# Optimization experiments

Measured on AMD Instinct MI355X. Metric: run time of the kernel, lower is better.

## Reference

```python
import jax, jax.numpy as jnp
import numpy as np

N, D, H, F = 384, 512, 8, 64  # n_nodes, in/out features, heads, per-head hidden
SLOPE = 0.2


def gat_v2_layer(x, mask, W_l, W_r, a):
    """GATv2 layer (is_concat=True). x: [N, D_in]; mask: [N, N, 1] bool.

    torch semantics: g_sum[i, j] = g_l[j] + g_r[i]; e = a . LeakyReLU(g_sum);
    softmax over j (dim=1); aggregate g_r with einsum('ijh,jhf->ihf').
    attn linear nn.Linear(F, 1) is shared across heads -> a: [F].
    """
    n = x.shape[0]
    g_l = (x @ W_l).reshape(n, H, F)
    g_r = (x @ W_r).reshape(n, H, F)
    # pairwise [i, j, h, f] = g_r[i] + g_l[j]  (the big O(N^2) intermediate)
    s = jax.nn.leaky_relu(g_r[:, None] + g_l[None, :], negative_slope=SLOPE)
    e = jnp.einsum('ijhf,f->ijh', s, a)
    e = jnp.where(mask, e, -jnp.inf)
    att = jax.nn.softmax(e, axis=1)  # normalize over source nodes j
    out = jnp.einsum('ijh,jhf->ihf', att, g_r)
    return out.reshape(n, H * F)


def setup_inputs() -> dict:
    key = jax.random.key(0)
    ks = jax.random.split(key, 8)
    x = jax.random.normal(ks[0], (N, D), dtype=jnp.float32)
    adj = jax.random.randint(ks[1], (N, N, 1), 0, 2, dtype=jnp.int32)
    sd = 1.0 / np.sqrt(D)
    sa = 1.0 / np.sqrt(F)
    W_l0 = jax.random.normal(ks[2], (D, H * F), dtype=jnp.float32) * sd
    W_r0 = jax.random.normal(ks[3], (D, H * F), dtype=jnp.float32) * sd
    a0 = jax.random.normal(ks[4], (F,), dtype=jnp.float32) * sa
    W_l1 = jax.random.normal(ks[5], (H * F, H * F), dtype=jnp.float32) * sd
    W_r1 = jax.random.normal(ks[6], (H * F, H * F), dtype=jnp.float32) * sd
    a1 = jax.random.normal(ks[7], (F,), dtype=jnp.float32) * sa
    return {"x": x, "adj": adj, "W_l0": W_l0, "W_r0": W_r0, "a0": a0,
            "W_l1": W_l1, "W_r1": W_r1, "a1": a1}


def reference(x, adj, W_l0, W_r0, a0, W_l1, W_r1, a1):
    n = x.shape[0]
    # selfloop: fill diagonal of adj with 1
    idx = jnp.arange(n)
    adj = adj.at[idx, idx, 0].set(1)
    mask = adj != 0  # [N, N, 1]
    # layer 0: GATv2 -> ELU (i < n_layers-1) -> residual
    out = jax.nn.elu(gat_v2_layer(x, mask, W_l0, W_r0, a0))
    x = x + out
    # layer 1: GATv2 -> Identity -> residual
    out = gat_v2_layer(x, mask, W_l1, W_r1, a1)
    x = x + out
    return x
```

## Files before the change

### kernel.cpp

```cpp
#include <hip/hip_runtime.h>
#include <hip/hip_bf16.h>
#include <stdint.h>

typedef unsigned short ushort_t;
typedef unsigned long long u64;
typedef __attribute__((ext_vector_type(8))) short short8;
typedef __attribute__((ext_vector_type(4))) float f32x4;

#define N_NODES 384
#define HF      512

__device__ inline ushort_t f2bf(float f) {
  __hip_bfloat16 b = __float2bfloat16(f);
  return *reinterpret_cast<ushort_t*>(&b);
}
__device__ inline float bf2f_u(ushort_t u) {
  union { float f; uint32_t i; } v; v.i = ((uint32_t)u) << 16; return v.f;
}

__global__ __launch_bounds__(256) void prep(
    const float* __restrict__ x, const int* __restrict__ adj,
    const float* __restrict__ w0, const float* __restrict__ w1,
    const float* __restrict__ w2, const float* __restrict__ w3,
    ushort_t* __restrict__ WT0, ushort_t* __restrict__ WT1,
    ushort_t* __restrict__ xb, u64* __restrict__ mbits)
{
  const int z = blockIdx.z;
  const int t = threadIdx.x;
  if (z == 4) {
    int idx = (blockIdx.y * 16 + blockIdx.x) * 256 + t;
#pragma unroll
    for (int r = 0; r < 3; ++r) {
      int i = idx + r * 65536;
      xb[i] = f2bf(x[i]);
    }
    return;
  }
  if (z == 5) {
    int b = blockIdx.y * 16 + blockIdx.x;
    if (b >= 96) return;
    int wave = t >> 6, lane = t & 63;
    int row = b * 4 + wave;
#pragma unroll
    for (int w = 0; w < 6; ++w) {
      int j = w * 64 + lane;
      int v = adj[row * N_NODES + j];
      u64 m = __ballot(v != 0 || row == j);
      if (lane == 0) mbits[row * 6 + w] = m;
    }
    return;
  }
  __shared__ ushort_t tile[32][33];
  const float* W = (z == 0) ? w0 : (z == 1) ? w1 : (z == 2) ? w2 : w3;
  ushort_t* WT = ((z < 2) ? WT0 : WT1) + (z & 1) * (512 * 512);
  const int n0 = blockIdx.x * 32, k0 = blockIdx.y * 32;
#pragma unroll
  for (int qq = 0; qq < 4; ++qq) {
    int idx = t + qq * 256, r = idx >> 5, c = idx & 31;
    tile[r][c] = f2bf(W[(k0 + r) * 512 + n0 + c]);
  }
  __syncthreads();
#pragma unroll
  for (int qq = 0; qq < 4; ++qq) {
    int idx = t + qq * 256, r = idx >> 5, c = idx & 31;
    WT[(n0 + r) * 512 + k0 + c] = tile[c][r];
  }
}

__global__ __launch_bounds__(256) void gemm_mfma(
    const ushort_t* __restrict__ A, const ushort_t* __restrict__ WT,
    float* __restrict__ G, ushort_t* __restrict__ glb,
    ushort_t* __restrict__ grT)
{
  const int t = threadIdx.x;
  const int wave = t >> 6, lane = t & 63;
  const int lm = lane & 15, q = lane >> 4;
  const int m0 = blockIdx.x * 16;
  const int n0 = (blockIdx.y * 4 + wave) * 32;

  const short8* Ap = (const short8*)A;
  const short8* Bp = (const short8*)WT;
  const int arow  = (m0 + lm) * 64 + q;
  const int brow0 = (n0 + lm) * 64 + q;
  const int brow1 = (n0 + 16 + lm) * 64 + q;

  f32x4 acc0 = {0.f, 0.f, 0.f, 0.f};
  f32x4 acc1 = {0.f, 0.f, 0.f, 0.f};
#pragma unroll
  for (int kc = 0; kc < 16; ++kc) {
    short8 af = Ap[arow  + kc * 4];
    short8 b0 = Bp[brow0 + kc * 4];
    short8 b1 = Bp[brow1 + kc * 4];
    acc0 = __builtin_amdgcn_mfma_f32_16x16x32_bf16(af, b0, acc0, 0, 0, 0);
    acc1 = __builtin_amdgcn_mfma_f32_16x16x32_bf16(af, b1, acc1, 0, 0, 0);
  }
  if (n0 < 512) {
#pragma unroll
    for (int r = 0; r < 4; ++r) {
      int m = m0 + q * 4 + r;
      glb[m * HF + n0 + lm]      = f2bf(acc0[r]);
      glb[m * HF + n0 + 16 + lm] = f2bf(acc1[r]);
    }
  } else {
#pragma unroll
    for (int r = 0; r < 4; ++r) {
      int m = m0 + q * 4 + r;
      G[m * 1024 + n0 + lm]      = acc0[r];
      G[m * 1024 + n0 + 16 + lm] = acc1[r];
    }
    int c0 = n0 - 512;
    uint2 p0, p1;
    p0.x = (uint32_t)f2bf(acc0[0]) | ((uint32_t)f2bf(acc0[1]) << 16);
    p0.y = (uint32_t)f2bf(acc0[2]) | ((uint32_t)f2bf(acc0[3]) << 16);
    p1.x = (uint32_t)f2bf(acc1[0]) | ((uint32_t)f2bf(acc1[1]) << 16);
    p1.y = (uint32_t)f2bf(acc1[2]) | ((uint32_t)f2bf(acc1[3]) << 16);
    *(uint2*)&grT[(c0 + lm) * 384 + m0 + q * 4]      = p0;
    *(uint2*)&grT[(c0 + 16 + lm) * 384 + m0 + q * 4] = p1;
  }
}

template <int LAYER>
__global__ __launch_bounds__(384) void attn_fused(
    const float* __restrict__ G, const ushort_t* __restrict__ glb,
    const ushort_t* __restrict__ grT, const u64* __restrict__ mbits,
    const float* __restrict__ resid_in, const float* __restrict__ avec,
    float* __restrict__ xcur_out, ushort_t* __restrict__ x1b_out,
    float* __restrict__ f_out)
{
  __shared__ __align__(16) char smem[55296];
  ushort_t (*s_gl)[72]      = (ushort_t(*)[72])smem;
  float    (*s_e)[N_NODES]  = (float(*)[N_NODES])smem;
  ushort_t (*s_pb)[392]     = (ushort_t(*)[392])(smem + 12288);
  __shared__ float s_bri[8];
  __shared__ u64   s_mask[8][6];

  const int t = threadIdx.x;
  const int i0 = blockIdx.x * 8, h = blockIdx.y;
  const int lane = t & 63, wave = t >> 6;

  if (t >= 256 && t < 304) ((u64*)s_mask)[t - 256] = mbits[i0 * 6 + (t - 256)];
  if (t >= 128 && t < 256) {
    int u = t - 128, il = u >> 4, fg = u & 15;
    float4 g4 = *(const float4*)(G + (i0 + il) * 1024 + 512 + h * 64 + fg * 4);
    float4 a4 = *(const float4*)(avec + fg * 4);
    float s = a4.x * g4.x + a4.y * g4.y + a4.z * g4.z + a4.w * g4.w;
    s += __shfl_xor(s, 1); s += __shfl_xor(s, 2);
    s += __shfl_xor(s, 4); s += __shfl_xor(s, 8);
    if (fg == 0) s_bri[il] = s;
  }
#pragma unroll
  for (int rep = 0; rep < 8; ++rep) {
    int idx = rep * 384 + t, row = idx >> 3, c = idx & 7;
    *(short8*)&s_gl[row][c * 8] =
        *(const short8*)&glb[row * HF + h * 64 + c * 8];
  }
  __syncthreads();

  float gl[64], av[64];
  {
    const short8* rowp = (const short8*)&s_gl[t][0];
#pragma unroll
    for (int c = 0; c < 8; ++c) {
      short8 v = rowp[c];
#pragma unroll
      for (int u2 = 0; u2 < 8; ++u2)
        gl[c * 8 + u2] = bf2f_u((ushort_t)v[u2]);
    }
#pragma unroll
    for (int c = 0; c < 16; ++c) {
      float4 a4 = ((const float4*)avec)[c];
      av[c * 4] = a4.x; av[c * 4 + 1] = a4.y;
      av[c * 4 + 2] = a4.z; av[c * 4 + 3] = a4.w;
    }
  }
  float accl = 0.f;
#pragma unroll
  for (int f = 0; f < 64; ++f) accl += av[f] * gl[f];
  __syncthreads();

  const int jw = t >> 6, jb = t & 63;
#pragma unroll
  for (int il = 0; il < 8; ++il) {
    const float4* gr4 = (const float4*)(G + (i0 + il) * 1024 + 512 + h * 64);
    float acc = 0.f;
#pragma unroll
    for (int c = 0; c < 16; ++c) {
      float4 g4 = gr4[c];
      acc += av[c * 4]     * fabsf(gl[c * 4]     + g4.x);
      acc += av[c * 4 + 1] * fabsf(gl[c * 4 + 1] + g4.y);
      acc += av[c * 4 + 2] * fabsf(gl[c * 4 + 2] + g4.z);
      acc += av[c * 4 + 3] * fabsf(gl[c * 4 + 3] + g4.w);
    }
    bool m = (s_mask[il][jw] >> jb) & 1;
    float e = 0.6f * (accl + s_bri[il]) + 0.4f * acc;
    s_e[il][t] = m ? e : -1e30f;
  }
  {
    ushort_t z0 = 0;
#pragma unroll
    for (int r8 = 0; r8 < 8; ++r8) s_pb[8 + r8][t] = z0;
  }
  __syncthreads();

  for (int il = wave; il < 8; il += 6) {
    float v[6];
    float mx = -1e30f;
#pragma unroll
    for (int c = 0; c < 6; ++c) { v[c] = s_e[il][lane + 64 * c]; mx = fmaxf(mx, v[c]); }
#pragma unroll
    for (int off = 32; off; off >>= 1) mx = fmaxf(mx, __shfl_xor(mx, off));
    float sum = 0.f;
#pragma unroll
    for (int c = 0; c < 6; ++c) { v[c] = __expf(v[c] - mx); sum += v[c]; }
#pragma unroll
    for (int off = 32; off; off >>= 1) sum += __shfl_xor(sum, off);
    float inv = 1.0f / sum;
#pragma unroll
    for (int c = 0; c < 6; ++c) s_pb[il][lane + 64 * c] = f2bf(v[c] * inv);
  }
  __syncthreads();

  if (t < 256) {
    const int lm = lane & 15, q = lane >> 4;
    const int f0 = wave * 16;
    const ushort_t* Brow = grT + (h * 64 + f0 + lm) * 384;
    f32x4 acc = {0.f, 0.f, 0.f, 0.f};
#pragma unroll
    for (int kc = 0; kc < 12; ++kc) {
      short8 af = *(const short8*)&s_pb[lm][kc * 32 + q * 8];
      short8 bf = *(const short8*)&Brow[kc * 32 + q * 8];
      acc = __builtin_amdgcn_mfma_f32_16x16x32_bf16(af, bf, acc, 0, 0, 0);
    }
    if (q < 2) {
#pragma unroll
      for (int r = 0; r < 4; ++r) {
        int i = i0 + q * 4 + r;
        int off = i * HF + h * 64 + f0 + lm;
        float o = acc[r];
        if (LAYER == 0) {
          float oe = (o > 0.f) ? o : (__expf(o) - 1.f);
          float vv = resid_in[off] + oe;
          xcur_out[off] = vv;
          x1b_out[off]  = f2bf(vv);
        } else {
          f_out[off] = resid_in[off] + o;
        }
      }
    }
  }
}

extern "C" void kernel_launch(void* const* d_in, const int* in_sizes, int n_in,
                              void* d_out, int out_size, void* d_ws, size_t ws_size,
                              hipStream_t stream) {
  const float* x   = (const float*)d_in[0];
  const int*   adj = (const int*)d_in[1];
  const float* Wl0 = (const float*)d_in[2];
  const float* Wr0 = (const float*)d_in[3];
  const float* a0  = (const float*)d_in[4];
  const float* Wl1 = (const float*)d_in[5];
  const float* Wr1 = (const float*)d_in[6];
  const float* a1  = (const float*)d_in[7];
  float* out = (float*)d_out;

  char* ws = (char*)d_ws;
  ushort_t* WT0  = (ushort_t*)(ws + 0L);
  ushort_t* WT1  = (ushort_t*)(ws + (1L << 20));
  ushort_t* xb   = (ushort_t*)(ws + (2L << 20));
  float*    G    = (float*)   (ws + (3L << 20));
  ushort_t* grT  = (ushort_t*)(ws + (5L << 20));
  ushort_t* x1b  = (ushort_t*)(ws + (6L << 20));
  ushort_t* glb  = (ushort_t*)(ws + (7L << 20));
  u64*      mbits= (u64*)     (ws + (8L << 20));
  float*    xcur = (float*)   (ws + (9L << 20));

  prep<<<dim3(16, 16, 6), 256, 0, stream>>>(x, adj, Wl0, Wr0, Wl1, Wr1,
                                            WT0, WT1, xb, mbits);
  gemm_mfma<<<dim3(24, 8), 256, 0, stream>>>(xb, WT0, G, glb, grT);
  attn_fused<0><<<dim3(48, 8), 384, 0, stream>>>(G, glb, grT, mbits, x, a0,
                                                 xcur, x1b, nullptr);
  gemm_mfma<<<dim3(24, 8), 256, 0, stream>>>(x1b, WT1, G, glb, grT);
  attn_fused<1><<<dim3(48, 8), 384, 0, stream>>>(G, glb, grT, mbits, xcur, a1,
                                                 nullptr, nullptr, out);
}
```

Before: 131.5 us.

## Fuse all stages into one persistent kernel with software grid barriers

Replaces the five separate launches (prep, two GEMMs, two attention kernels) with a single persistent kernel of 256 blocks. The stages are separated by atomic-counter grid barriers, and a small init kernel resets the counters. The attention tile grows from 8 to 12 rows so 256 blocks cover the work, and the GEMM is remapped to 3 waves per block. This removes per-launch overhead and inter-kernel gaps. In exchange it relies on all 256 blocks being co-resident and adds spin-barrier cost, and larger attention tiles mean fewer blocks run in parallel.

```diff
diff --git a/kernel.cpp b/kernel.cpp
--- a/kernel.cpp
+++ b/kernel.cpp
@@ -9,6 +9,8 @@
 
 #define N_NODES 384
 #define HF      512
+#define IT      12
+#define NBLK    256
 
 __device__ inline ushort_t f2bf(float f) {
   __hip_bfloat16 b = __float2bfloat16(f);
@@ -18,128 +20,93 @@
   union { float f; uint32_t i; } v; v.i = ((uint32_t)u) << 16; return v.f;
 }
 
-__global__ __launch_bounds__(256) void prep(
-    const float* __restrict__ x, const int* __restrict__ adj,
-    const float* __restrict__ w0, const float* __restrict__ w1,
-    const float* __restrict__ w2, const float* __restrict__ w3,
-    ushort_t* __restrict__ WT0, ushort_t* __restrict__ WT1,
-    ushort_t* __restrict__ xb, u64* __restrict__ mbits)
+__global__ void init_bar(unsigned* bar) {
+  if (threadIdx.x < 8) bar[threadIdx.x] = 0;
+}
+
+__device__ __forceinline__ void gridbar(unsigned* cnt) {
+  __threadfence();
+  __syncthreads();
+  if (threadIdx.x == 0) {
+    if (atomicAdd(cnt, 1u) + 1u < NBLK) {
+      while (__hip_atomic_load(cnt, __ATOMIC_RELAXED,
+                               __HIP_MEMORY_SCOPE_AGENT) < NBLK) {
+        __builtin_amdgcn_s_sleep(2);
+      }
+    }
+    __threadfence();
+  }
+  __syncthreads();
+}
+
+__device__ __forceinline__ void gemm_phase(
+    const ushort_t* A, const ushort_t* WT,
+    float* G, ushort_t* glb, ushort_t* grT)
 {
-  const int z = blockIdx.z;
-  const int t = threadIdx.x;
-  if (z == 4) {
-    int idx = (blockIdx.y * 16 + blockIdx.x) * 256 + t;
-#pragma unroll
-    for (int r = 0; r < 3; ++r) {
-      int i = idx + r * 65536;
-      xb[i] = f2bf(x[i]);
-    }
-    return;
-  }
-  if (z == 5) {
-    int b = blockIdx.y * 16 + blockIdx.x;
-    if (b >= 96) return;
-    int wave = t >> 6, lane = t & 63;
-    int row = b * 4 + wave;
-#pragma unroll
-    for (int w = 0; w < 6; ++w) {
-      int j = w * 64 + lane;
-      int v = adj[row * N_NODES + j];
-      u64 m = __ballot(v != 0 || row == j);
-      if (lane == 0) mbits[row * 6 + w] = m;
-    }
-    return;
-  }
-  __shared__ ushort_t tile[32][33];
-  const float* W = (z == 0) ? w0 : (z == 1) ? w1 : (z == 2) ? w2 : w3;
-  ushort_t* WT = ((z < 2) ? WT0 : WT1) + (z & 1) * (512 * 512);
-  const int n0 = blockIdx.x * 32, k0 = blockIdx.y * 32;
-#pragma unroll
-  for (int qq = 0; qq < 4; ++qq) {
-    int idx = t + qq * 256, r = idx >> 5, c = idx & 31;
-    tile[r][c] = f2bf(W[(k0 + r) * 512 + n0 + c]);
-  }
-  __syncthreads();
-#pragma unroll
-  for (int qq = 0; qq < 4; ++qq) {
-    int idx = t + qq * 256, r = idx >> 5, c = idx & 31;
-    WT[(n0 + r) * 512 + k0 + c] = tile[c][r];
-  }
-}
-
-__global__ __launch_bounds__(256) void gemm_mfma(
-    const ushort_t* __restrict__ A, const ushort_t* __restrict__ WT,
-    float* __restrict__ G, ushort_t* __restrict__ glb,
-    ushort_t* __restrict__ grT)
+  const int t = threadIdx.x, wave = t >> 6, lane = t & 63;
+  if (wave < 3) {
+    const int u = blockIdx.x * 3 + wave;
+    const int m0 = (u >> 5) * 16;
+    const int n0 = (u & 31) * 32;
+    const int lm = lane & 15, q = lane >> 4;
+
+    const short8* Ap = (const short8*)A;
+    const short8* Bp = (const short8*)WT;
+    const int arow  = (m0 + lm) * 64 + q;
+    const int brow0 = (n0 + lm) * 64 + q;
+    const int brow1 = (n0 + 16 + lm) * 64 + q;
+
+    f32x4 acc0 = {0.f, 0.f, 0.f, 0.f};
+    f32x4 acc1 = {0.f, 0.f, 0.f, 0.f};
+#pragma unroll
+    for (int kc = 0; kc < 16; ++kc) {
+      short8 af = Ap[arow  + kc * 4];
+      short8 b0 = Bp[brow0 + kc * 4];
+      short8 b1 = Bp[brow1 + kc * 4];
+      acc0 = __builtin_amdgcn_mfma_f32_16x16x32_bf16(af, b0, acc0, 0, 0, 0);
+      acc1 = __builtin_amdgcn_mfma_f32_16x16x32_bf16(af, b1, acc1, 0, 0, 0);
+    }
+    if (n0 < 512) {
+#pragma unroll
+      for (int r = 0; r < 4; ++r) {
+        int m = m0 + q * 4 + r;
+        glb[m * HF + n0 + lm]      = f2bf(acc0[r]);
+        glb[m * HF + n0 + 16 + lm] = f2bf(acc1[r]);
+      }
+    } else {
+#pragma unroll
+      for (int r = 0; r < 4; ++r) {
+        int m = m0 + q * 4 + r;
+        G[m * 1024 + n0 + lm]      = acc0[r];
+        G[m * 1024 + n0 + 16 + lm] = acc1[r];
+      }
+      int c0 = n0 - 512;
+      uint2 p0, p1;
+      p0.x = (uint32_t)f2bf(acc0[0]) | ((uint32_t)f2bf(acc0[1]) << 16);
+      p0.y = (uint32_t)f2bf(acc0[2]) | ((uint32_t)f2bf(acc0[3]) << 16);
+      p1.x = (uint32_t)f2bf(acc1[0]) | ((uint32_t)f2bf(acc1[1]) << 16);
+      p1.y = (uint32_t)f2bf(acc1[2]) | ((uint32_t)f2bf(acc1[3]) << 16);
+      *(uint2*)&grT[(c0 + lm) * 384 + m0 + q * 4]      = p0;
+      *(uint2*)&grT[(c0 + 16 + lm) * 384 + m0 + q * 4] = p1;
+    }
+  }
+}
+
+__device__ __forceinline__ void attn_phase(int layer,
+    const float* G, const ushort_t* glb, const ushort_t* grT,
+    const u64* mbits, const float* resid, const float* avec,
+    float* xcur, ushort_t* x1b, float* fout,
+    char* smem, float* s_bri, u64 (*s_mask)[6])
 {
-  const int t = threadIdx.x;
-  const int wave = t >> 6, lane = t & 63;
-  const int lm = lane & 15, q = lane >> 4;
-  const int m0 = blockIdx.x * 16;
-  const int n0 = (blockIdx.y * 4 + wave) * 32;
-
-  const short8* Ap = (const short8*)A;
-  const short8* Bp = (const short8*)WT;
-  const int arow  = (m0 + lm) * 64 + q;
-  const int brow0 = (n0 + lm) * 64 + q;
-  const int brow1 = (n0 + 16 + lm) * 64 + q;
-
-  f32x4 acc0 = {0.f, 0.f, 0.f, 0.f};
-  f32x4 acc1 = {0.f, 0.f, 0.f, 0.f};
-#pragma unroll
-  for (int kc = 0; kc < 16; ++kc) {
-    short8 af = Ap[arow  + kc * 4];
-    short8 b0 = Bp[brow0 + kc * 4];
-    short8 b1 = Bp[brow1 + kc * 4];
-    acc0 = __builtin_amdgcn_mfma_f32_16x16x32_bf16(af, b0, acc0, 0, 0, 0);
-    acc1 = __builtin_amdgcn_mfma_f32_16x16x32_bf16(af, b1, acc1, 0, 0, 0);
-  }
-  if (n0 < 512) {
-#pragma unroll
-    for (int r = 0; r < 4; ++r) {
-      int m = m0 + q * 4 + r;
-      glb[m * HF + n0 + lm]      = f2bf(acc0[r]);
-      glb[m * HF + n0 + 16 + lm] = f2bf(acc1[r]);
-    }
-  } else {
-#pragma unroll
-    for (int r = 0; r < 4; ++r) {
-      int m = m0 + q * 4 + r;
-      G[m * 1024 + n0 + lm]      = acc0[r];
-      G[m * 1024 + n0 + 16 + lm] = acc1[r];
-    }
-    int c0 = n0 - 512;
-    uint2 p0, p1;
-    p0.x = (uint32_t)f2bf(acc0[0]) | ((uint32_t)f2bf(acc0[1]) << 16);
-    p0.y = (uint32_t)f2bf(acc0[2]) | ((uint32_t)f2bf(acc0[3]) << 16);
-    p1.x = (uint32_t)f2bf(acc1[0]) | ((uint32_t)f2bf(acc1[1]) << 16);
-    p1.y = (uint32_t)f2bf(acc1[2]) | ((uint32_t)f2bf(acc1[3]) << 16);
-    *(uint2*)&grT[(c0 + lm) * 384 + m0 + q * 4]      = p0;
-    *(uint2*)&grT[(c0 + 16 + lm) * 384 + m0 + q * 4] = p1;
-  }
-}
-
-template <int LAYER>
-__global__ __launch_bounds__(384) void attn_fused(
-    const float* __restrict__ G, const ushort_t* __restrict__ glb,
-    const ushort_t* __restrict__ grT, const u64* __restrict__ mbits,
-    const float* __restrict__ resid_in, const float* __restrict__ avec,
-    float* __restrict__ xcur_out, ushort_t* __restrict__ x1b_out,
-    float* __restrict__ f_out)
-{
-  __shared__ __align__(16) char smem[55296];
-  ushort_t (*s_gl)[72]      = (ushort_t(*)[72])smem;
-  float    (*s_e)[N_NODES]  = (float(*)[N_NODES])smem;
-  ushort_t (*s_pb)[392]     = (ushort_t(*)[392])(smem + 12288);
-  __shared__ float s_bri[8];
-  __shared__ u64   s_mask[8][6];
-
-  const int t = threadIdx.x;
-  const int i0 = blockIdx.x * 8, h = blockIdx.y;
-  const int lane = t & 63, wave = t >> 6;
-
-  if (t >= 256 && t < 304) ((u64*)s_mask)[t - 256] = mbits[i0 * 6 + (t - 256)];
-  if (t >= 128 && t < 256) {
+  ushort_t (*s_gl)[72]     = (ushort_t(*)[72])smem;
+  float    (*s_e)[N_NODES] = (float(*)[N_NODES])smem;
+  ushort_t (*s_pb)[392]    = (ushort_t(*)[392])(smem + 18432);
+
+  const int t = threadIdx.x, lane = t & 63, wave = t >> 6;
+  const int i0 = (blockIdx.x >> 3) * IT, h = blockIdx.x & 7;
+
+  if (t < 72) ((u64*)s_mask)[t] = mbits[i0 * 6 + t];
+  if (t >= 128 && t < 320) {
     int u = t - 128, il = u >> 4, fg = u & 15;
     float4 g4 = *(const float4*)(G + (i0 + il) * 1024 + 512 + h * 64 + fg * 4);
     float4 a4 = *(const float4*)(avec + fg * 4);
@@ -180,7 +147,7 @@
 
   const int jw = t >> 6, jb = t & 63;
 #pragma unroll
-  for (int il = 0; il < 8; ++il) {
+  for (int il = 0; il < IT; ++il) {
     const float4* gr4 = (const float4*)(G + (i0 + il) * 1024 + 512 + h * 64);
     float acc = 0.f;
 #pragma unroll
@@ -195,14 +162,11 @@
     float e = 0.6f * (accl + s_bri[il]) + 0.4f * acc;
     s_e[il][t] = m ? e : -1e30f;
   }
-  {
-    ushort_t z0 = 0;
-#pragma unroll
-    for (int r8 = 0; r8 < 8; ++r8) s_pb[8 + r8][t] = z0;
-  }
-  __syncthreads();
-
-  for (int il = wave; il < 8; il += 6) {
+#pragma unroll
+  for (int r4 = 0; r4 < 4; ++r4) s_pb[IT + r4][t] = 0;
+  __syncthreads();
+
+  for (int il = wave; il < IT; il += 6) {
     float v[6];
     float mx = -1e30f;
 #pragma unroll
@@ -220,7 +184,7 @@
   }
   __syncthreads();
 
-  if (t < 256) {
+  if (wave < 4) {
     const int lm = lane & 15, q = lane >> 4;
     const int f0 = wave * 16;
     const ushort_t* Brow = grT + (h * 64 + f0 + lm) * 384;
@@ -231,23 +195,97 @@
       short8 bf = *(const short8*)&Brow[kc * 32 + q * 8];
       acc = __builtin_amdgcn_mfma_f32_16x16x32_bf16(af, bf, acc, 0, 0, 0);
     }
-    if (q < 2) {
+    if (q < 3) {
 #pragma unroll
       for (int r = 0; r < 4; ++r) {
         int i = i0 + q * 4 + r;
         int off = i * HF + h * 64 + f0 + lm;
         float o = acc[r];
-        if (LAYER == 0) {
+        if (layer == 0) {
           float oe = (o > 0.f) ? o : (__expf(o) - 1.f);
-          float vv = resid_in[off] + oe;
-          xcur_out[off] = vv;
-          x1b_out[off]  = f2bf(vv);
+          float vv = resid[off] + oe;
+          xcur[off] = vv;
+          x1b[off]  = f2bf(vv);
         } else {
-          f_out[off] = resid_in[off] + o;
+          fout[off] = resid[off] + o;
         }
       }
     }
   }
+}
+
+__global__ __launch_bounds__(384) void mega(
+    const float* __restrict__ x, const int* __restrict__ adj,
+    const float* __restrict__ Wl0, const float* __restrict__ Wr0,
+    const float* __restrict__ a0,  const float* __restrict__ Wl1,
+    const float* __restrict__ Wr1, const float* __restrict__ a1,
+    float* out, ushort_t* WT0, ushort_t* WT1, ushort_t* xb,
+    float* G, ushort_t* glb, ushort_t* grT, ushort_t* x1b,
+    u64* mbits, float* xcur, unsigned* bar)
+{
+  __shared__ __align__(16) char smem[55296];
+  __shared__ float s_bri[IT];
+  __shared__ u64   s_mask[IT][6];
+
+  const int t = threadIdx.x, b = blockIdx.x;
+  const int lane = t & 63, wave = t >> 6;
+
+  {
+    ushort_t (*tile)[33] = (ushort_t(*)[33])smem;
+    for (int rep = 0; rep < 4; ++rep) {
+      int tau = b * 4 + rep;
+      int z = tau >> 8, tid = tau & 255;
+      const float* W = (z == 0) ? Wl0 : (z == 1) ? Wr0 : (z == 2) ? Wl1 : Wr1;
+      ushort_t* WT = ((z < 2) ? WT0 : WT1) + (z & 1) * (512 * 512);
+      int n0 = (tid & 15) * 32, k0 = (tid >> 4) * 32;
+      if (t < 256) {
+#pragma unroll
+        for (int qq = 0; qq < 4; ++qq) {
+          int idx = t + qq * 256, r = idx >> 5, c = idx & 31;
+          tile[r][c] = f2bf(W[(k0 + r) * 512 + n0 + c]);
+        }
+      }
+      __syncthreads();
+      if (t < 256) {
+#pragma unroll
+        for (int qq = 0; qq < 4; ++qq) {
+          int idx = t + qq * 256, r = idx >> 5, c = idx & 31;
+          WT[(n0 + r) * 512 + k0 + c] = tile[c][r];
+        }
+      }
+      __syncthreads();
+    }
+  }
+#pragma unroll
+  for (int r = 0; r < 2; ++r) {
+    int i = b * 768 + r * 384 + t;
+    xb[i] = f2bf(x[i]);
+  }
+  {
+    int row = b;
+    int j = wave * 64 + lane;
+    u64 m = __ballot(adj[row * N_NODES + j] != 0 || row == j);
+    if (lane == 0) mbits[row * 6 + wave] = m;
+    if (b < 128) {
+      row = 256 + b;
+      m = __ballot(adj[row * N_NODES + j] != 0 || row == j);
+      if (lane == 0) mbits[row * 6 + wave] = m;
+    }
+  }
+  gridbar(bar + 0);
+
+  gemm_phase(xb, WT0, G, glb, grT);
+  gridbar(bar + 1);
+
+  attn_phase(0, G, glb, grT, mbits, x, a0, xcur, x1b, out,
+             smem, s_bri, s_mask);
+  gridbar(bar + 2);
+
+  gemm_phase(x1b, WT1, G, glb, grT);
+  gridbar(bar + 3);
+
+  attn_phase(1, G, glb, grT, mbits, xcur, a1, xcur, x1b, out,
+             smem, s_bri, s_mask);
 }
 
 extern "C" void kernel_launch(void* const* d_in, const int* in_sizes, int n_in,
@@ -273,13 +311,10 @@
   ushort_t* glb  = (ushort_t*)(ws + (7L << 20));
   u64*      mbits= (u64*)     (ws + (8L << 20));
   float*    xcur = (float*)   (ws + (9L << 20));
-
-  prep<<<dim3(16, 16, 6), 256, 0, stream>>>(x, adj, Wl0, Wr0, Wl1, Wr1,
-                                            WT0, WT1, xb, mbits);
-  gemm_mfma<<<dim3(24, 8), 256, 0, stream>>>(xb, WT0, G, glb, grT);
-  attn_fused<0><<<dim3(48, 8), 384, 0, stream>>>(G, glb, grT, mbits, x, a0,
-                                                 xcur, x1b, nullptr);
-  gemm_mfma<<<dim3(24, 8), 256, 0, stream>>>(x1b, WT1, G, glb, grT);
-  attn_fused<1><<<dim3(48, 8), 384, 0, stream>>>(G, glb, grT, mbits, xcur, a1,
-                                                 nullptr, nullptr, out);
-}
+  unsigned* bar  = (unsigned*)(ws + (10L << 20));
+
+  init_bar<<<1, 64, 0, stream>>>(bar);
+  mega<<<NBLK, 384, 0, stream>>>(x, adj, Wl0, Wr0, a0, Wl1, Wr1, a1, out,
+                                 WT0, WT1, xb, G, glb, grT, x1b, mbits,
+                                 xcur, bar);
+}
```

New measurement: 297.4 us. 2.26x slower.

## Drop prep kernel: convert weights in GEMM, fuse mask build, retile attention rows

Applied to the files above, without the earlier changes.

Removes the separate prep kernel. The GEMM now reads fp32 X and the untransposed fp32 weights directly and packs them to bf16 in registers, and the layer-0 GEMM also builds the adjacency bitmask. The attention kernel handles 12 target rows per block instead of 8, which cuts the grid from 48x8 to 32x8, and it no longer writes a bf16 copy of the residual. This saves one launch and the transpose/convert traffic, but the GEMM B loads become strided per-element fp32 reads with repeated conversion work, and the mask build is serialized onto some GEMM blocks.

```diff
diff --git a/kernel.cpp b/kernel.cpp
--- a/kernel.cpp
+++ b/kernel.cpp
@@ -9,6 +9,7 @@
 
 #define N_NODES 384
 #define HF      512
+#define IT      12
 
 __device__ inline ushort_t f2bf(float f) {
   __hip_bfloat16 b = __float2bfloat16(f);
@@ -17,80 +18,44 @@
 __device__ inline float bf2f_u(ushort_t u) {
   union { float f; uint32_t i; } v; v.i = ((uint32_t)u) << 16; return v.f;
 }
-
-__global__ __launch_bounds__(256) void prep(
-    const float* __restrict__ x, const int* __restrict__ adj,
-    const float* __restrict__ w0, const float* __restrict__ w1,
-    const float* __restrict__ w2, const float* __restrict__ w3,
-    ushort_t* __restrict__ WT0, ushort_t* __restrict__ WT1,
-    ushort_t* __restrict__ xb, u64* __restrict__ mbits)
+__device__ inline short8 pack8(const float* s) {
+  short8 r;
+#pragma unroll
+  for (int j = 0; j < 8; ++j) r[j] = (short)f2bf(s[j]);
+  return r;
+}
+
+__global__ __launch_bounds__(256) void gemm_direct(
+    const float* __restrict__ X, const float* __restrict__ WL,
+    const float* __restrict__ WR, float* __restrict__ G,
+    ushort_t* __restrict__ glb, ushort_t* __restrict__ grT,
+    const int* __restrict__ adj, u64* __restrict__ mbits)
 {
-  const int z = blockIdx.z;
-  const int t = threadIdx.x;
-  if (z == 4) {
-    int idx = (blockIdx.y * 16 + blockIdx.x) * 256 + t;
-#pragma unroll
-    for (int r = 0; r < 3; ++r) {
-      int i = idx + r * 65536;
-      xb[i] = f2bf(x[i]);
-    }
-    return;
-  }
-  if (z == 5) {
-    int b = blockIdx.y * 16 + blockIdx.x;
-    if (b >= 96) return;
-    int wave = t >> 6, lane = t & 63;
-    int row = b * 4 + wave;
-#pragma unroll
-    for (int w = 0; w < 6; ++w) {
-      int j = w * 64 + lane;
-      int v = adj[row * N_NODES + j];
-      u64 m = __ballot(v != 0 || row == j);
-      if (lane == 0) mbits[row * 6 + w] = m;
-    }
-    return;
-  }
-  __shared__ ushort_t tile[32][33];
-  const float* W = (z == 0) ? w0 : (z == 1) ? w1 : (z == 2) ? w2 : w3;
-  ushort_t* WT = ((z < 2) ? WT0 : WT1) + (z & 1) * (512 * 512);
-  const int n0 = blockIdx.x * 32, k0 = blockIdx.y * 32;
-#pragma unroll
-  for (int qq = 0; qq < 4; ++qq) {
-    int idx = t + qq * 256, r = idx >> 5, c = idx & 31;
-    tile[r][c] = f2bf(W[(k0 + r) * 512 + n0 + c]);
-  }
-  __syncthreads();
-#pragma unroll
-  for (int qq = 0; qq < 4; ++qq) {
-    int idx = t + qq * 256, r = idx >> 5, c = idx & 31;
-    WT[(n0 + r) * 512 + k0 + c] = tile[c][r];
-  }
-}
-
-__global__ __launch_bounds__(256) void gemm_mfma(
-    const ushort_t* __restrict__ A, const ushort_t* __restrict__ WT,
-    float* __restrict__ G, ushort_t* __restrict__ glb,
-    ushort_t* __restrict__ grT)
-{
-  const int t = threadIdx.x;
-  const int wave = t >> 6, lane = t & 63;
+  const int t = threadIdx.x, wave = t >> 6, lane = t & 63;
   const int lm = lane & 15, q = lane >> 4;
   const int m0 = blockIdx.x * 16;
   const int n0 = (blockIdx.y * 4 + wave) * 32;
-
-  const short8* Ap = (const short8*)A;
-  const short8* Bp = (const short8*)WT;
-  const int arow  = (m0 + lm) * 64 + q;
-  const int brow0 = (n0 + lm) * 64 + q;
-  const int brow1 = (n0 + 16 + lm) * 64 + q;
+  const float* Wp = (n0 < 512) ? (WL + n0) : (WR + (n0 - 512));
+  const float* Arow = X + (m0 + lm) * HF;
 
   f32x4 acc0 = {0.f, 0.f, 0.f, 0.f};
   f32x4 acc1 = {0.f, 0.f, 0.f, 0.f};
-#pragma unroll
+#pragma unroll 4
   for (int kc = 0; kc < 16; ++kc) {
-    short8 af = Ap[arow  + kc * 4];
-    short8 b0 = Bp[brow0 + kc * 4];
-    short8 b1 = Bp[brow1 + kc * 4];
+    const int kbase = kc * 32 + q * 8;
+    float4 a0 = *(const float4*)(Arow + kbase);
+    float4 a1 = *(const float4*)(Arow + kbase + 4);
+    float av8[8] = {a0.x, a0.y, a0.z, a0.w, a1.x, a1.y, a1.z, a1.w};
+    short8 af = pack8(av8);
+    float b0f[8], b1f[8];
+#pragma unroll
+    for (int j = 0; j < 8; ++j) {
+      const float* r = Wp + (kbase + j) * HF;
+      b0f[j] = r[lm];
+      b1f[j] = r[16 + lm];
+    }
+    short8 b0 = pack8(b0f);
+    short8 b1 = pack8(b1f);
     acc0 = __builtin_amdgcn_mfma_f32_16x16x32_bf16(af, b0, acc0, 0, 0, 0);
     acc1 = __builtin_amdgcn_mfma_f32_16x16x32_bf16(af, b1, acc1, 0, 0, 0);
   }
@@ -117,6 +82,18 @@
     *(uint2*)&grT[(c0 + lm) * 384 + m0 + q * 4]      = p0;
     *(uint2*)&grT[(c0 + 16 + lm) * 384 + m0 + q * 4] = p1;
   }
+  if (adj != nullptr && blockIdx.y == 0) {
+    int rbase = (blockIdx.x * 4 + wave) * 4;
+    for (int rr = 0; rr < 4; ++rr) {
+      int row = rbase + rr;
+#pragma unroll
+      for (int w = 0; w < 6; ++w) {
+        int j = w * 64 + lane;
+        u64 m = __ballot(adj[row * N_NODES + j] != 0 || row == j);
+        if (lane == 0) mbits[row * 6 + w] = m;
+      }
+    }
+  }
 }
 
 template <int LAYER>
@@ -124,22 +101,21 @@
     const float* __restrict__ G, const ushort_t* __restrict__ glb,
     const ushort_t* __restrict__ grT, const u64* __restrict__ mbits,
     const float* __restrict__ resid_in, const float* __restrict__ avec,
-    float* __restrict__ xcur_out, ushort_t* __restrict__ x1b_out,
-    float* __restrict__ f_out)
+    float* __restrict__ xcur_out, float* __restrict__ f_out)
 {
   __shared__ __align__(16) char smem[55296];
-  ushort_t (*s_gl)[72]      = (ushort_t(*)[72])smem;
-  float    (*s_e)[N_NODES]  = (float(*)[N_NODES])smem;
-  ushort_t (*s_pb)[392]     = (ushort_t(*)[392])(smem + 12288);
-  __shared__ float s_bri[8];
-  __shared__ u64   s_mask[8][6];
+  ushort_t (*s_gl)[72]     = (ushort_t(*)[72])smem;
+  float    (*s_e)[N_NODES] = (float(*)[N_NODES])smem;
+  ushort_t (*s_pb)[392]    = (ushort_t(*)[392])(smem + 18432);
+  __shared__ float s_bri[IT];
+  __shared__ u64   s_mask[IT][6];
 
   const int t = threadIdx.x;
-  const int i0 = blockIdx.x * 8, h = blockIdx.y;
+  const int i0 = blockIdx.x * IT, h = blockIdx.y;
   const int lane = t & 63, wave = t >> 6;
 
-  if (t >= 256 && t < 304) ((u64*)s_mask)[t - 256] = mbits[i0 * 6 + (t - 256)];
-  if (t >= 128 && t < 256) {
+  if (t < 72) ((u64*)s_mask)[t] = mbits[i0 * 6 + t];
+  if (t >= 128 && t < 320) {
     int u = t - 128, il = u >> 4, fg = u & 15;
     float4 g4 = *(const float4*)(G + (i0 + il) * 1024 + 512 + h * 64 + fg * 4);
     float4 a4 = *(const float4*)(avec + fg * 4);
@@ -180,7 +156,7 @@
 
   const int jw = t >> 6, jb = t & 63;
 #pragma unroll
-  for (int il = 0; il < 8; ++il) {
+  for (int il = 0; il < IT; ++il) {
     const float4* gr4 = (const float4*)(G + (i0 + il) * 1024 + 512 + h * 64);
     float acc = 0.f;
 #pragma unroll
@@ -195,14 +171,11 @@
     float e = 0.6f * (accl + s_bri[il]) + 0.4f * acc;
     s_e[il][t] = m ? e : -1e30f;
   }
-  {
-    ushort_t z0 = 0;
-#pragma unroll
-    for (int r8 = 0; r8 < 8; ++r8) s_pb[8 + r8][t] = z0;
-  }
-  __syncthreads();
-
-  for (int il = wave; il < 8; il += 6) {
+#pragma unroll
+  for (int r4 = 0; r4 < 4; ++r4) s_pb[IT + r4][t] = 0;
+  __syncthreads();
+
+  for (int il = wave; il < IT; il += 6) {
     float v[6];
     float mx = -1e30f;
 #pragma unroll
@@ -220,7 +193,7 @@
   }
   __syncthreads();
 
-  if (t < 256) {
+  if (wave < 4) {
     const int lm = lane & 15, q = lane >> 4;
     const int f0 = wave * 16;
     const ushort_t* Brow = grT + (h * 64 + f0 + lm) * 384;
@@ -231,7 +204,7 @@
       short8 bf = *(const short8*)&Brow[kc * 32 + q * 8];
       acc = __builtin_amdgcn_mfma_f32_16x16x32_bf16(af, bf, acc, 0, 0, 0);
     }
-    if (q < 2) {
+    if (q < 3) {
 #pragma unroll
       for (int r = 0; r < 4; ++r) {
         int i = i0 + q * 4 + r;
@@ -239,9 +212,7 @@
         float o = acc[r];
         if (LAYER == 0) {
           float oe = (o > 0.f) ? o : (__expf(o) - 1.f);
-          float vv = resid_in[off] + oe;
-          xcur_out[off] = vv;
-          x1b_out[off]  = f2bf(vv);
+          xcur_out[off] = resid_in[off] + oe;
         } else {
           f_out[off] = resid_in[off] + o;
         }
@@ -264,22 +235,18 @@
   float* out = (float*)d_out;
 
   char* ws = (char*)d_ws;
-  ushort_t* WT0  = (ushort_t*)(ws + 0L);
-  ushort_t* WT1  = (ushort_t*)(ws + (1L << 20));
-  ushort_t* xb   = (ushort_t*)(ws + (2L << 20));
-  float*    G    = (float*)   (ws + (3L << 20));
-  ushort_t* grT  = (ushort_t*)(ws + (5L << 20));
-  ushort_t* x1b  = (ushort_t*)(ws + (6L << 20));
-  ushort_t* glb  = (ushort_t*)(ws + (7L << 20));
-  u64*      mbits= (u64*)     (ws + (8L << 20));
-  float*    xcur = (float*)   (ws + (9L << 20));
-
-  prep<<<dim3(16, 16, 6), 256, 0, stream>>>(x, adj, Wl0, Wr0, Wl1, Wr1,
-                                            WT0, WT1, xb, mbits);
-  gemm_mfma<<<dim3(24, 8), 256, 0, stream>>>(xb, WT0, G, glb, grT);
-  attn_fused<0><<<dim3(48, 8), 384, 0, stream>>>(G, glb, grT, mbits, x, a0,
-                                                 xcur, x1b, nullptr);
-  gemm_mfma<<<dim3(24, 8), 256, 0, stream>>>(x1b, WT1, G, glb, grT);
-  attn_fused<1><<<dim3(48, 8), 384, 0, stream>>>(G, glb, grT, mbits, xcur, a1,
-                                                 nullptr, nullptr, out);
-}
+  float*    G    = (float*)   (ws + 0L);
+  ushort_t* grT  = (ushort_t*)(ws + (2L << 20));
+  ushort_t* glb  = (ushort_t*)(ws + (3L << 20));
+  u64*      mbits= (u64*)     (ws + (4L << 20));
+  float*    xcur = (float*)   (ws + (5L << 20));
+
+  gemm_direct<<<dim3(24, 8), 256, 0, stream>>>(x, Wl0, Wr0, G, glb, grT,
+                                               adj, mbits);
+  attn_fused<0><<<dim3(32, 8), 384, 0, stream>>>(G, glb, grT, mbits, x, a0,
+                                                 xcur, nullptr);
+  gemm_direct<<<dim3(24, 8), 256, 0, stream>>>(xcur, Wl1, Wr1, G, glb, grT,
+                                               nullptr, nullptr);
+  attn_fused<1><<<dim3(32, 8), 384, 0, stream>>>(G, glb, grT, mbits, xcur, a1,
+                                                 nullptr, out);
+}
```

New measurement: 124.1 us. 5.6% less time.
